# Performance work log

Hardware: AMD Instinct MI355X
Metric: run time of the kernel (lower is better)

## Reference

```python
import jax, jax.numpy as jnp
import numpy as np

ND, NP, NS = 30000, 30000, 10000
HID, NH = 128, 8
HD = HID // NH  # 16
E_DD = E_DP = E_PD = E_PP = 1000000
E_SD = 500000
NEG_SLOPE = 0.2  # DGL GATConv default leaky_relu slope


def _gat(x_src, x_dst, src, dst, W, al, ar, b):
    """Single-relation GATConv (DGL semantics, eval mode / no dropout)."""
    n_dst = x_dst.shape[0]
    z_src = (x_src @ W).reshape(-1, NH, HD)   # [Ns,H,D]
    z_dst = (x_dst @ W).reshape(-1, NH, HD)   # [Nd,H,D]
    el = jnp.sum(z_src * al, axis=-1)          # [Ns,H]
    er = jnp.sum(z_dst * ar, axis=-1)          # [Nd,H]
    e = jax.nn.leaky_relu(el[src] + er[dst], NEG_SLOPE)  # [E,H]
    # edge softmax over incoming edges of each dst node
    emax = jax.ops.segment_max(e, dst, num_segments=n_dst)
    emax = jnp.where(jnp.isfinite(emax), emax, 0.0)
    ex = jnp.exp(e - emax[dst])
    den = jax.ops.segment_sum(ex, dst, num_segments=n_dst)
    attn = ex / jnp.maximum(den[dst], 1e-9)    # [E,H]
    msg = attn[:, :, None] * z_src[src]        # [E,H,D]
    out = jax.ops.segment_sum(msg, dst, num_segments=n_dst)  # [Nd,H,D]
    return out + b.reshape(1, NH, HD)


def _semantic(feats, W1, b1, W2, b2):
    # feats: [N,R,HID]; per-node softmax over relation axis
    s = jnp.tanh(feats @ W1 + b1) @ W2 + b2    # [N,R,1]
    w = jax.nn.softmax(s, axis=1)
    return jnp.sum(feats * w, axis=1)          # [N,HID]


def setup_inputs() -> dict:
    key = jax.random.key(0)
    ks = jax.random.split(key, 40)
    it = iter(range(40))
    def nrm(shape, scale=1.0):
        return jax.random.normal(ks[next(it)], shape, dtype=jnp.float32) * scale
    sc = 1.0 / float(np.sqrt(HID))
    inp = {}
    inp["h_drug"] = nrm((ND, HID))
    inp["h_protein"] = nrm((NP, HID))
    inp["h_se"] = nrm((NS, HID))
    for rel in ["dd", "dp", "pd", "pp", "sd"]:
        inp[f"W_{rel}"] = nrm((HID, HID), sc)
        inp[f"al_{rel}"] = nrm((NH, HD), sc)
        inp[f"ar_{rel}"] = nrm((NH, HD), sc)
        inp[f"b_{rel}"] = jnp.zeros((HID,), dtype=jnp.float32)
    inp["W1"] = nrm((HID, HID), sc)
    inp["b1"] = jnp.zeros((HID,), dtype=jnp.float32)
    inp["W2"] = nrm((HID, 1), sc)
    inp["b2"] = jnp.zeros((1,), dtype=jnp.float32)
    def ridx(n, e):
        return jax.random.randint(ks[next(it)], (e,), 0, n, dtype=jnp.int32)
    inp["src_dd"] = ridx(ND, E_DD); inp["dst_dd"] = ridx(ND, E_DD)
    inp["src_dp"] = ridx(ND, E_DP); inp["dst_dp"] = ridx(NP, E_DP)
    inp["src_pd"] = ridx(NP, E_PD); inp["dst_pd"] = ridx(ND, E_PD)
    inp["src_pp"] = ridx(NP, E_PP); inp["dst_pp"] = ridx(NP, E_PP)
    inp["src_sd"] = ridx(NS, E_SD); inp["dst_sd"] = ridx(ND, E_SD)
    return inp


def reference(h_drug, h_protein, h_se,
              W_dd, al_dd, ar_dd, b_dd, W_dp, al_dp, ar_dp, b_dp,
              W_pd, al_pd, ar_pd, b_pd, W_pp, al_pp, ar_pp, b_pp,
              W_sd, al_sd, ar_sd, b_sd, W1, b1, W2, b2,
              src_dd, dst_dd, src_dp, dst_dp, src_pd, dst_pd,
              src_pp, dst_pp, src_sd, dst_sd):
    # per-relation GAT message passing (HeteroGraphConv, aggregate='stack')
    o_dd = _gat(h_drug, h_drug, src_dd, dst_dd, W_dd, al_dd, ar_dd, b_dd)
    o_pd = _gat(h_protein, h_drug, src_pd, dst_pd, W_pd, al_pd, ar_pd, b_pd)
    o_sd = _gat(h_se, h_drug, src_sd, dst_sd, W_sd, al_sd, ar_sd, b_sd)
    o_dp = _gat(h_drug, h_protein, src_dp, dst_dp, W_dp, al_dp, ar_dp, b_dp)
    o_pp = _gat(h_protein, h_protein, src_pp, dst_pp, W_pp, al_pp, ar_pp, b_pp)
    drug_stack = jnp.stack([o_dd, o_pd, o_sd], axis=1).reshape(ND, 3, HID)
    prot_stack = jnp.stack([o_dp, o_pp], axis=1).reshape(NP, 2, HID)
    out_drug = _semantic(drug_stack, W1, b1, W2, b2)
    out_protein = _semantic(prot_stack, W1, b1, W2, b2)
    return out_drug, out_protein
```

## Files before the change

### kernel.cpp

```cpp
#include <hip/hip_runtime.h>
#include <hip/hip_bf16.h>

typedef unsigned short u16;
typedef __attribute__((ext_vector_type(8))) short short8;
typedef __attribute__((ext_vector_type(4))) float f32x4;

#define ND 30000
#define NP 30000
#define NS 10000
#define CSTRIDE 30016
#define ETOT 4500000
#define CHUNK 4608
#define NC 977
#define NBR 118
#define NB 590

__device__ __forceinline__ float bf2f(u16 u) {
  union { unsigned int i; float f; } c; c.i = ((unsigned int)u) << 16; return c.f;
}
__device__ __forceinline__ u16 f2bf(float f) {
  union { float f; unsigned int i; } c; c.f = f;
  unsigned int u = c.i;
  unsigned int r = (u + 0x7fffu + ((u >> 16) & 1u)) >> 16;
  return (u16)r;
}

__global__ void k_detect(const void* x, int* flag) {
  if (threadIdx.x == 0 && blockIdx.x == 0) {
    const u16* p = (const u16*)x;
    int sane = 0;
    for (int i = 0; i < 256; ++i) {
      const u16 v = p[2 * i];
      const int e = (v >> 7) & 0xff;
      sane += (e >= 100 && e <= 140) ? 1 : 0;
    }
    *flag = (sane >= 200) ? 1 : 0;
  }
}

__device__ __forceinline__ float ld_in(const void* p, int i, int isbf) {
  return isbf ? bf2f(((const u16*)p)[i]) : ((const float*)p)[i];
}

struct PJobs { const void* W[5]; const void* al[5]; const void* ar[5];
               float* wal[5]; float* war[5]; };
__global__ __launch_bounds__(128) void k_prep_all(PJobs J, const int* flagp) {
  const int b = blockIdx.x;
  const int k = threadIdx.x;
  const int isbf = *flagp;
  for (int h = 0; h < 8; ++h) {
    float sa = 0.f, sr = 0.f;
    for (int d = 0; d < 16; ++d) {
      const float wv = ld_in(J.W[b], k * 128 + h * 16 + d, isbf);
      sa = fmaf(wv, ld_in(J.al[b], h * 16 + d, isbf), sa);
      sr = fmaf(wv, ld_in(J.ar[b], h * 16 + d, isbf), sr);
    }
    J.wal[b][h * 128 + k] = sa;
    J.war[b][h * 128 + k] = sr;
  }
}

struct KPack { const void* W[6]; const float* wal[6]; const float* war[6];
               u16* out[6]; };
__global__ __launch_bounds__(256) void k_pack_all(KPack J, const int* flagp) {
  const int job = blockIdx.x / 9;
  const int i0 = (blockIdx.x % 9) * 2048 + threadIdx.x * 8;
  const int isbf = *flagp;
  const int kc = i0 / 4608;
  const int rem = i0 - kc * 4608;
  const int n = rem >> 5;
  const int q = (rem >> 3) & 3;
  u16 vals[8];
  #pragma unroll
  for (int j = 0; j < 8; ++j) {
    const int k = kc * 32 + q * 8 + j;
    float v;
    if (job == 5)      v = (n < 128) ? ld_in(J.W[5], k * 128 + n, isbf) : 0.f;
    else if (n < 128)  v = ld_in(J.W[job], k * 128 + n, isbf);
    else if (n < 136)  v = J.wal[job][(n - 128) * 128 + k];
    else               v = J.war[job][(n - 136) * 128 + k];
    vals[j] = f2bf(v);
  }
  *(uint4*)&J.out[job][i0] = *(uint4*)vals;
}

struct XJobs {
  const void* x[8]; const u16* bp[8]; u16* z[8]; float* el[8]; float* er[8];
  int N[8]; int t0[8]; int blk0[9];
};
__global__ __launch_bounds__(256) void k_xform_all(XJobs J, const int* flagp) {
  __shared__ __align__(16) u16 Bf[18432];
  __shared__ __align__(16) u16 As[64 * 136];
  const int tid = threadIdx.x;
  const int isbf = *flagp;

  int job = 0, b = blockIdx.x;
  while (b >= J.blk0[job + 1]) ++job;
  const int row0 = (b - J.blk0[job]) * 64;
  const int N = J.N[job];
  const int t0 = J.t0[job];
  const u16* bp = J.bp[job];
  const void* x = J.x[job];

  if (t0 == 0) {
    for (int i = tid * 8; i < 18432; i += 2048)
      *(uint4*)&Bf[i] = *(const uint4*)&bp[i];
  } else {
    const int i = tid * 8;
    const int kc = i >> 9;
    const int off = (kc * 144 + 128) * 32 + (i & 511);
    *(uint4*)&Bf[off] = *(const uint4*)&bp[off];
  }

  if (isbf) {
    const uint4* xv = (const uint4*)x;
    for (int i = tid; i < 1024; i += 256) {
      const int r = i >> 4, c8 = i & 15;
      const int row = row0 + r;
      uint4 v = make_uint4(0, 0, 0, 0);
      if (row < N) v = xv[row * 16 + c8];
      *(uint4*)&As[r * 136 + c8 * 8] = v;
    }
  } else {
    const float4* xf = (const float4*)x;
    for (int i = tid; i < 2048; i += 256) {
      const int r = i >> 5, c4 = i & 31;
      const int row = row0 + r;
      unsigned long long pk = 0ull;
      if (row < N) {
        const float4 v = xf[row * 32 + c4];
        pk = (unsigned long long)f2bf(v.x) | ((unsigned long long)f2bf(v.y) << 16)
           | ((unsigned long long)f2bf(v.z) << 32) | ((unsigned long long)f2bf(v.w) << 48);
      }
      *(unsigned long long*)&As[r * 136 + c4 * 4] = pk;
    }
  }
  __syncthreads();

  const int wave = tid >> 6;
  const int lane = tid & 63;
  const int q = lane >> 4;
  const int c = lane & 15;

  f32x4 accT[8];
  f32x4 acc8 = (f32x4){0.f, 0.f, 0.f, 0.f};
  if (t0 == 0) {
    #pragma unroll
    for (int t = 0; t < 8; ++t) accT[t] = (f32x4){0.f, 0.f, 0.f, 0.f};
  }

  #pragma unroll
  for (int kc = 0; kc < 4; ++kc) {
    const short8 a = *(const short8*)&As[(wave * 16 + c) * 136 + kc * 32 + q * 8];
    if (t0 == 0) {
      #pragma unroll
      for (int t = 0; t < 8; ++t) {
        const short8 bb = *(const short8*)&Bf[((kc * 144 + t * 16 + c) * 4 + q) * 8];
        accT[t] = __builtin_amdgcn_mfma_f32_16x16x32_bf16(a, bb, accT[t], 0, 0, 0);
      }
    }
    const short8 b8 = *(const short8*)&Bf[((kc * 144 + 128 + c) * 4 + q) * 8];
    acc8 = __builtin_amdgcn_mfma_f32_16x16x32_bf16(a, b8, acc8, 0, 0, 0);
  }

  const int rbase = row0 + wave * 16 + q * 4;
  if (t0 == 0 && J.z[job]) {
    u16* zo = J.z[job];
    #pragma unroll
    for (int t = 0; t < 8; ++t)
      #pragma unroll
      for (int r = 0; r < 4; ++r) {
        const int row = rbase + r;
        if (row < N) zo[row * 128 + t * 16 + c] = f2bf(accT[t][r]);
      }
  }
  #pragma unroll
  for (int r = 0; r < 4; ++r) {
    const int row = rbase + r;
    if (row < N) {
      const float v = acc8[r];
      if (c < 8) { if (J.el[job]) J.el[job][row * 8 + c] = v; }
      else       { if (J.er[job]) J.er[job][row * 8 + (c - 8)] = v; }
    }
  }
}

struct EJobs { const int* src[5]; const int* dst[5]; };
__device__ __forceinline__ int e_job(int e) {
  return (e >= 1000000) + (e >= 2000000) + (e >= 2500000) + (e >= 3500000);
}
__device__ __forceinline__ int e_base(int j) {
  const int base[6] = {0, 1000000, 2000000, 2500000, 3500000, 4500000};
  return base[j];
}

__global__ __launch_bounds__(256) void k_hist(EJobs J, int* __restrict__ ghist) {
  __shared__ int h[NB];
  const int c = blockIdx.x, tid = threadIdx.x;
  for (int i = tid; i < NB; i += 256) h[i] = 0;
  __syncthreads();
  const int e0 = c * CHUNK;
  #pragma unroll
  for (int t = 0; t < 18; ++t) {
    const int e = e0 + t * 256 + tid;
    if (e < ETOT) {
      const int j = e_job(e);
      const int d = J.dst[j][e - e_base(j)];
      atomicAdd(&h[j * NBR + (d >> 8)], 1);
    }
  }
  __syncthreads();
  for (int i = tid; i < NB; i += 256) ghist[c * NB + i] = h[i];
}

__global__ __launch_bounds__(256) void k_bucketscan(
    const int* __restrict__ ghist, int* __restrict__ gcur, int* __restrict__ totals)
{
  __shared__ int ts[256];
  const int b = blockIdx.x, tid = threadIdx.x;
  int v[4]; int sum = 0;
  #pragma unroll
  for (int i = 0; i < 4; ++i) {
    const int c = tid * 4 + i;
    v[i] = (c < NC) ? ghist[c * NB + b] : 0;
    sum += v[i];
  }
  ts[tid] = sum;
  __syncthreads();
  for (int o = 1; o < 256; o <<= 1) {
    const int x = (tid >= o) ? ts[tid - o] : 0;
    __syncthreads();
    ts[tid] += x;
    __syncthreads();
  }
  int run = (tid == 0) ? 0 : ts[tid - 1];
  #pragma unroll
  for (int i = 0; i < 4; ++i) {
    const int c = tid * 4 + i;
    if (c < NC) gcur[b * NC + c] = run;
    run += v[i];
  }
  if (tid == 255) totals[b] = ts[255];
}

__global__ __launch_bounds__(1024) void k_base(
    const int* __restrict__ totals, int* __restrict__ base)
{
  __shared__ int ts[1024];
  const int tid = threadIdx.x;
  ts[tid] = (tid < NB) ? totals[tid] : 0;
  __syncthreads();
  for (int o = 1; o < 1024; o <<= 1) {
    const int x = (tid >= o) ? ts[tid - o] : 0;
    __syncthreads();
    ts[tid] += x;
    __syncthreads();
  }
  if (tid < NB) base[tid] = (tid == 0) ? 0 : ts[tid - 1];
  if (tid == 0) base[NB] = ETOT;
}

__global__ __launch_bounds__(256) void k_bin(
    EJobs J, const int* __restrict__ gcur, const int* __restrict__ base,
    unsigned int* __restrict__ bin)
{
  __shared__ int cur[NB];
  const int c = blockIdx.x, tid = threadIdx.x;
  for (int i = tid; i < NB; i += 256) cur[i] = base[i] + gcur[i * NC + c];
  __syncthreads();
  const int e0 = c * CHUNK;
  #pragma unroll
  for (int t = 0; t < 18; ++t) {
    const int e = e0 + t * 256 + tid;
    if (e < ETOT) {
      const int j = e_job(e);
      const int le = e - e_base(j);
      const int d = J.dst[j][le];
      const int s = J.src[j][le];
      const int p = atomicAdd(&cur[j * NBR + (d >> 8)], 1);
      bin[p] = ((unsigned int)(d & 255) << 16) | (unsigned int)s;
    }
  }
}

__global__ __launch_bounds__(256) void k_fill2(
    const unsigned int* __restrict__ bin, const int* __restrict__ base,
    u16* __restrict__ csr, int* __restrict__ offsets)
{
  __shared__ int cnt[256], curs[256];
  const int b = blockIdx.x, tid = threadIdx.x;
  const int rel = b / NBR;
  const int bloc = b - rel * NBR;
  const int d0 = bloc << 8;
  const int gbeg = base[b];
  const int n = base[b + 1] - gbeg;
  cnt[tid] = 0;
  __syncthreads();
  for (int i = tid; i < n; i += 256)
    atomicAdd(&cnt[bin[gbeg + i] >> 16], 1);
  __syncthreads();
  const int orig = cnt[tid];
  for (int o = 1; o < 256; o <<= 1) {
    const int x = (tid >= o) ? cnt[tid - o] : 0;
    __syncthreads();
    cnt[tid] += x;
    __syncthreads();
  }
  const int ex = cnt[tid] - orig;
  curs[tid] = ex;
  const int ebr = e_base(rel);
  const int d = d0 + tid;
  if (d < 30000) offsets[rel * CSTRIDE + d] = (gbeg - ebr) + ex;
  if (bloc == NBR - 1 && tid == 0)
    offsets[rel * CSTRIDE + 30000] = e_base(rel + 1) - ebr;
  __syncthreads();
  for (int i = tid; i < n; i += 256) {
    const unsigned int v = bin[gbeg + i];
    const int p = atomicAdd(&curs[v >> 16], 1);
    csr[gbeg + p] = (u16)(v & 0xffffu);
  }
}

struct AJobs { const u16* csr[5]; const int* off[5]; const float* el[5];
               const float* er[5]; const u16* z[5]; const void* b[5];
               u16* feats[5]; int stride[5]; };
__global__ __launch_bounds__(256) void k_agg_all(AJobs J, const int* flagp) {
  const int gw = (blockIdx.x * 256 + threadIdx.x) >> 6;
  if (gw >= 150000) return;
  const int job = gw / 30000;
  const int d = gw - job * 30000;
  const int lane = threadIdx.x & 63;
  const int h = lane >> 3;
  const float* el = J.el[job];
  const u16* z = J.z[job];
  const u16* csr = J.csr[job];
  const float erh = J.er[job][d * 8 + h];
  const int beg = J.off[job][d];
  const int end = J.off[job][d + 1];
  const int zoff = lane * 2;

  float a0 = 0.f, a1 = 0.f, b0 = 0.f, b1 = 0.f, dA = 0.f, dB = 0.f;
  int p = beg;
  for (; p + 4 <= end; p += 4) {
    const int s0 = csr[p];
    const int s1 = csr[p + 1];
    const int s2 = csr[p + 2];
    const int s3 = csr[p + 3];
    float e0 = el[s0 * 8 + h] + erh;
    float e1 = el[s1 * 8 + h] + erh;
    float e2 = el[s2 * 8 + h] + erh;
    float e3 = el[s3 * 8 + h] + erh;
    const unsigned int z0 = *(const unsigned int*)(z + s0 * 128 + zoff);
    const unsigned int z1 = *(const unsigned int*)(z + s1 * 128 + zoff);
    const unsigned int z2 = *(const unsigned int*)(z + s2 * 128 + zoff);
    const unsigned int z3 = *(const unsigned int*)(z + s3 * 128 + zoff);
    e0 = fminf((e0 >= 0.f) ? e0 : 0.2f * e0, 60.f);
    e1 = fminf((e1 >= 0.f) ? e1 : 0.2f * e1, 60.f);
    e2 = fminf((e2 >= 0.f) ? e2 : 0.2f * e2, 60.f);
    e3 = fminf((e3 >= 0.f) ? e3 : 0.2f * e3, 60.f);
    const float x0 = __expf(e0);
    const float x1 = __expf(e1);
    const float x2 = __expf(e2);
    const float x3 = __expf(e3);
    dA += x0 + x2;
    dB += x1 + x3;
    a0 = fmaf(x0, bf2f((u16)(z0 & 0xffffu)), a0);
    a1 = fmaf(x0, bf2f((u16)(z0 >> 16)), a1);
    b0 = fmaf(x1, bf2f((u16)(z1 & 0xffffu)), b0);
    b1 = fmaf(x1, bf2f((u16)(z1 >> 16)), b1);
    a0 = fmaf(x2, bf2f((u16)(z2 & 0xffffu)), a0);
    a1 = fmaf(x2, bf2f((u16)(z2 >> 16)), a1);
    b0 = fmaf(x3, bf2f((u16)(z3 & 0xffffu)), b0);
    b1 = fmaf(x3, bf2f((u16)(z3 >> 16)), b1);
  }
  for (; p < end; ++p) {
    const int s0 = csr[p];
    float e0 = el[s0 * 8 + h] + erh;
    e0 = fminf((e0 >= 0.f) ? e0 : 0.2f * e0, 60.f);
    const float x0 = __expf(e0);
    const unsigned int z0 = *(const unsigned int*)(z + s0 * 128 + zoff);
    dA += x0;
    a0 = fmaf(x0, bf2f((u16)(z0 & 0xffffu)), a0);
    a1 = fmaf(x0, bf2f((u16)(z0 >> 16)), a1);
  }
  const float inv = 1.f / fmaxf(dA + dB, 1e-9f);
  const int isbf = *flagp;
  const int j0 = lane * 2;
  const float v0 = (a0 + b0) * inv + ld_in(J.b[job], j0, isbf);
  const float v1 = (a1 + b1) * inv + ld_in(J.b[job], j0 + 1, isbf);
  const unsigned int packed = (unsigned int)f2bf(v0) | ((unsigned int)f2bf(v1) << 16);
  *(unsigned int*)(J.feats[job] + d * J.stride[job] + j0) = packed;
}

__global__ __launch_bounds__(256) void k_sem_all(
    const u16* __restrict__ f, const u16* __restrict__ w1pack,
    const void* __restrict__ b1, const void* __restrict__ W2,
    const void* __restrict__ b2, float* __restrict__ s_out, int total,
    const int* __restrict__ flagp)
{
  __shared__ __align__(16) u16 Bf[18432];
  __shared__ __align__(16) u16 As[64 * 136];
  __shared__ float b1S[128], W2S[128];
  const int tid = threadIdx.x;
  const int isbf = *flagp;
  const int row0 = blockIdx.x * 64;

  for (int i = tid * 8; i < 18432; i += 2048)
    *(uint4*)&Bf[i] = *(const uint4*)&w1pack[i];
  if (tid < 128) { b1S[tid] = ld_in(b1, tid, isbf); W2S[tid] = ld_in(W2, tid, isbf); }
  {
    const uint4* xv = (const uint4*)f;
    for (int i = tid; i < 1024; i += 256) {
      const int r = i >> 4, c8 = i & 15;
      const int row = row0 + r;
      uint4 v = make_uint4(0, 0, 0, 0);
      if (row < total) v = xv[row * 16 + c8];
      *(uint4*)&As[r * 136 + c8 * 8] = v;
    }
  }
  __syncthreads();

  const int wave = tid >> 6;
  const int lane = tid & 63;
  const int q = lane >> 4;
  const int c = lane & 15;

  f32x4 acc[8];
  #pragma unroll
  for (int t = 0; t < 8; ++t) acc[t] = (f32x4){0.f, 0.f, 0.f, 0.f};

  #pragma unroll
  for (int kc = 0; kc < 4; ++kc) {
    const short8 a = *(const short8*)&As[(wave * 16 + c) * 136 + kc * 32 + q * 8];
    #pragma unroll
    for (int t = 0; t < 8; ++t) {
      const short8 bb = *(const short8*)&Bf[((kc * 144 + t * 16 + c) * 4 + q) * 8];
      acc[t] = __builtin_amdgcn_mfma_f32_16x16x32_bf16(a, bb, acc[t], 0, 0, 0);
    }
  }

  float part[4] = {0.f, 0.f, 0.f, 0.f};
  #pragma unroll
  for (int t = 0; t < 8; ++t) {
    const int n = t * 16 + c;
    const float b1v = b1S[n];
    const float w2v = W2S[n];
    #pragma unroll
    for (int r = 0; r < 4; ++r) {
      const float hv = acc[t][r] + b1v;
      const float e = __expf(2.f * hv);
      const float th = 1.f - 2.f / (e + 1.f);
      part[r] = fmaf(th, w2v, part[r]);
    }
  }
  #pragma unroll
  for (int r = 0; r < 4; ++r) {
    part[r] += __shfl_xor(part[r], 1);
    part[r] += __shfl_xor(part[r], 2);
    part[r] += __shfl_xor(part[r], 4);
    part[r] += __shfl_xor(part[r], 8);
  }
  if (c == 0) {
    const float b2v = ld_in(b2, 0, isbf);
    #pragma unroll
    for (int r = 0; r < 4; ++r) {
      const int row = row0 + wave * 16 + q * 4 + r;
      if (row < total) s_out[row] = part[r] + b2v;
    }
  }
}

__global__ __launch_bounds__(256) void k_combine_all(
    const u16* __restrict__ feats, const float* __restrict__ s,
    void* __restrict__ out, const int* __restrict__ flagp)
{
  const int i = blockIdx.x * 256 + threadIdx.x;
  if (i >= 7680000) return;
  const int isbf = *flagp;
  const bool drug = (i < 3840000);
  const int li = drug ? i : i - 3840000;
  const int n = li >> 7;
  const int j = li & 127;
  const float* sr = s + (drug ? n * 3 : 90000 + n * 2);
  const u16* fb = feats + (drug ? n * 384 : 11520000 + n * 256);
  const float s0v = sr[0];
  const float s1v = sr[1];
  const float s2v = drug ? sr[2] : -3.4e38f;
  const float m = fmaxf(fmaxf(s0v, s1v), s2v);
  const float w0 = __expf(s0v - m);
  const float w1 = __expf(s1v - m);
  const float w2 = drug ? __expf(s2v - m) : 0.f;
  const float inv = 1.f / (w0 + w1 + w2);
  float acc = w0 * bf2f(fb[j]) + w1 * bf2f(fb[128 + j]);
  if (drug) acc += w2 * bf2f(fb[256 + j]);
  const float v = acc * inv;
  if (isbf) ((u16*)out)[i] = f2bf(v);
  else      ((float*)out)[i] = v;
}

extern "C" void kernel_launch(void* const* d_in, const int* in_sizes, int n_in,
                              void* d_out, int out_size, void* d_ws, size_t ws_size,
                              hipStream_t stream)
{
  (void)in_sizes; (void)n_in; (void)out_size; (void)ws_size;

  const void* h_drug = d_in[0];
  const void* h_prot = d_in[1];
  const void* h_se   = d_in[2];
  const void* W_dd = d_in[3];  const void* al_dd = d_in[4];
  const void* ar_dd = d_in[5]; const void* b_dd  = d_in[6];
  const void* W_dp = d_in[7];  const void* al_dp = d_in[8];
  const void* ar_dp = d_in[9]; const void* b_dp  = d_in[10];
  const void* W_pd = d_in[11]; const void* al_pd = d_in[12];
  const void* ar_pd = d_in[13];const void* b_pd  = d_in[14];
  const void* W_pp = d_in[15]; const void* al_pp = d_in[16];
  const void* ar_pp = d_in[17];const void* b_pp  = d_in[18];
  const void* W_sd = d_in[19]; const void* al_sd = d_in[20];
  const void* ar_sd = d_in[21];const void* b_sd  = d_in[22];
  const void* W1 = d_in[23];   const void* b1 = d_in[24];
  const void* W2 = d_in[25];   const void* b2 = d_in[26];
  const int* src_dd = (const int*)d_in[27];
  const int* dst_dd = (const int*)d_in[28];
  const int* src_dp = (const int*)d_in[29];
  const int* dst_dp = (const int*)d_in[30];
  const int* src_pd = (const int*)d_in[31];
  const int* dst_pd = (const int*)d_in[32];
  const int* src_pp = (const int*)d_in[33];
  const int* dst_pp = (const int*)d_in[34];
  const int* src_sd = (const int*)d_in[35];
  const int* dst_sd = (const int*)d_in[36];

  char* w = (char*)d_ws;
  float* el5   = (float*)(w);
  float* er5   = (float*)(w + 4800000);
  u16* z_dd    = (u16*)(w + 9600000);
  u16* z_pd    = (u16*)(w + 17280000);
  u16* z_sd    = (u16*)(w + 24960000);
  u16* z_dp    = (u16*)(w + 27520000);
  u16* z_pp    = (u16*)(w + 35200000);
  int* offsets = (int*)(w + 42880000);
  u16* csr     = (u16*)(w + 43480320);
  int* ghist   = (int*)(w + 52480320);
  int* gcur    = (int*)(w + 54786048);
  int* basep   = (int*)(w + 57091776);
  float* s     = (float*)(w + 57094144);
  u16* feats   = (u16*)(w + 57694144);
  unsigned int* bin = (unsigned int*)(w + 57694144);
  int* flag    = (int*)(w + 96094144);
  float* ww    = (float*)(w + 96094160);
  u16* packs   = (u16*)(w + 96135120);

  float *wal[5], *war[5];
  for (int r = 0; r < 5; ++r) { wal[r] = ww + r * 2048; war[r] = ww + r * 2048 + 1024; }
  u16* pk[6];
  for (int r = 0; r < 6; ++r) pk[r] = packs + r * 18432;
  float* el_r[5]; float* er_r[5];
  for (int r = 0; r < 5; ++r) { el_r[r] = el5 + r * 240000; er_r[r] = er5 + r * 240000; }
  u16* feats_d = feats;
  u16* feats_p = feats + 11520000;

  const dim3 blk(256);

  k_detect<<<dim3(1), dim3(64), 0, stream>>>(h_drug, flag);

  PJobs pj;
  pj.W[0]=W_dd; pj.al[0]=al_dd; pj.ar[0]=ar_dd;
  pj.W[1]=W_pd; pj.al[1]=al_pd; pj.ar[1]=ar_pd;
  pj.W[2]=W_sd; pj.al[2]=al_sd; pj.ar[2]=ar_sd;
  pj.W[3]=W_dp; pj.al[3]=al_dp; pj.ar[3]=ar_dp;
  pj.W[4]=W_pp; pj.al[4]=al_pp; pj.ar[4]=ar_pp;
  for (int r = 0; r < 5; ++r) { pj.wal[r] = wal[r]; pj.war[r] = war[r]; }
  k_prep_all<<<dim3(5), dim3(128), 0, stream>>>(pj, flag);

  KPack kp;
  kp.W[0]=W_dd; kp.W[1]=W_pd; kp.W[2]=W_sd; kp.W[3]=W_dp; kp.W[4]=W_pp; kp.W[5]=W1;
  for (int r = 0; r < 5; ++r) { kp.wal[r] = wal[r]; kp.war[r] = war[r]; }
  kp.wal[5]=nullptr; kp.war[5]=nullptr;
  for (int r = 0; r < 6; ++r) kp.out[r] = pk[r];
  k_pack_all<<<dim3(54), blk, 0, stream>>>(kp, flag);

  EJobs ej;
  ej.src[0]=src_dd; ej.dst[0]=dst_dd;
  ej.src[1]=src_pd; ej.dst[1]=dst_pd;
  ej.src[2]=src_sd; ej.dst[2]=dst_sd;
  ej.src[3]=src_dp; ej.dst[3]=dst_dp;
  ej.src[4]=src_pp; ej.dst[4]=dst_pp;
  k_hist<<<dim3(NC), blk, 0, stream>>>(ej, ghist);
  k_bucketscan<<<dim3(NB), blk, 0, stream>>>(ghist, gcur, basep + NB + 1);
  k_base<<<dim3(1), dim3(1024), 0, stream>>>(basep + NB + 1, basep);
  k_bin<<<dim3(NC), blk, 0, stream>>>(ej, gcur, basep, bin);
  k_fill2<<<dim3(NB), blk, 0, stream>>>(bin, basep, csr, offsets);

  XJobs xj;
  auto setx = [&](int i, const void* x, const u16* bp, u16* z, float* el,
                  float* er, int N, int t0) {
    xj.x[i]=x; xj.bp[i]=bp; xj.z[i]=z; xj.el[i]=el; xj.er[i]=er; xj.N[i]=N; xj.t0[i]=t0;
  };
  setx(0, h_drug, pk[0], z_dd, el_r[0], er_r[0], ND, 0);
  setx(1, h_prot, pk[1], z_pd, el_r[1], nullptr, NP, 0);
  setx(2, h_drug, pk[1], nullptr, nullptr, er_r[1], ND, 8);
  setx(3, h_se,   pk[2], z_sd, el_r[2], nullptr, NS, 0);
  setx(4, h_drug, pk[2], nullptr, nullptr, er_r[2], ND, 8);
  setx(5, h_drug, pk[3], z_dp, el_r[3], nullptr, ND, 0);
  setx(6, h_prot, pk[3], nullptr, nullptr, er_r[3], NP, 8);
  setx(7, h_prot, pk[4], z_pp, el_r[4], er_r[4], NP, 0);
  {
    int acc = 0;
    for (int i = 0; i < 8; ++i) { xj.blk0[i] = acc; acc += (xj.N[i] + 63) / 64; }
    xj.blk0[8] = acc;
    k_xform_all<<<dim3(acc), blk, 0, stream>>>(xj, flag);
  }

  AJobs aj;
  const int ebase[5] = {0, 1000000, 2000000, 2500000, 3500000};
  const void* bias[5] = {b_dd, b_pd, b_sd, b_dp, b_pp};
  u16* fb[5] = {feats_d, feats_d + 128, feats_d + 256, feats_p, feats_p + 128};
  const int fstride[5] = {384, 384, 384, 256, 256};
  const u16* zz[5] = {z_dd, z_pd, z_sd, z_dp, z_pp};
  for (int r = 0; r < 5; ++r) {
    aj.csr[r] = csr + ebase[r];
    aj.off[r] = offsets + r * CSTRIDE;
    aj.el[r] = el_r[r];
    aj.er[r] = er_r[r];
    aj.z[r] = zz[r];
    aj.b[r] = bias[r];
    aj.feats[r] = fb[r];
    aj.stride[r] = fstride[r];
  }
  k_agg_all<<<dim3(150000 / 4), blk, 0, stream>>>(aj, flag);

  k_sem_all<<<dim3((150000 + 63) / 64), blk, 0, stream>>>(feats, pk[5], b1, W2, b2, s, 150000, flag);
  k_combine_all<<<dim3((7680000 + 255) / 256), blk, 0, stream>>>(feats, s, d_out, flag);
}
```

Baseline: 608.1 us.

## Merge preprocessing launches, inline dtype detection, and cooperatively gather edges in aggregation

Cuts the kernel count by merging independent stages into shared launches: prep with hist, pack with bucketscan, and fill2 with xform. The separate base-scan kernel is dropped; each consumer block recomputes the base offsets from the totals. Every kernel now detects the input dtype itself with a ballot instead of reading a flag written by a one-thread kernel. The aggregation kernel changes so each lane computes the attention exp for one of eight edges, then shares the source index and weight through readlane and bpermute. The histogram chunk size doubles, halving the number of blocks. The cost is redundant detection and scan work in every block, plus extra shared memory in the merged kernels.

```diff
diff --git a/kernel.cpp b/kernel.cpp
--- a/kernel.cpp
+++ b/kernel.cpp
@@ -10,8 +10,8 @@
 #define NS 10000
 #define CSTRIDE 30016
 #define ETOT 4500000
-#define CHUNK 4608
-#define NC 977
+#define CHUNK 9216
+#define NC 489
 #define NBR 118
 #define NB 590
 
@@ -25,29 +25,37 @@
   return (u16)r;
 }
 
-__global__ void k_detect(const void* x, int* flag) {
-  if (threadIdx.x == 0 && blockIdx.x == 0) {
-    const u16* p = (const u16*)x;
-    int sane = 0;
-    for (int i = 0; i < 256; ++i) {
-      const u16 v = p[2 * i];
-      const int e = (v >> 7) & 0xff;
-      sane += (e >= 100 && e <= 140) ? 1 : 0;
-    }
-    *flag = (sane >= 200) ? 1 : 0;
-  }
+__device__ __forceinline__ int detect_isbf(const void* x) {
+  __shared__ int cnt4[4];
+  const int tid = threadIdx.x;
+  const u16 v = ((const u16*)x)[2 * tid];
+  const int e = (v >> 7) & 0xff;
+  const unsigned long long m = __ballot(e >= 100 && e <= 140);
+  if ((tid & 63) == 0) cnt4[tid >> 6] = __popcll(m);
+  __syncthreads();
+  const int sane = cnt4[0] + cnt4[1] + cnt4[2] + cnt4[3];
+  return sane >= 200;
 }
 
 __device__ __forceinline__ float ld_in(const void* p, int i, int isbf) {
   return isbf ? bf2f(((const u16*)p)[i]) : ((const float*)p)[i];
 }
 
+struct EJobs { const int* src[5]; const int* dst[5]; };
+__device__ __forceinline__ int e_job(int e) {
+  return (e >= 1000000) + (e >= 2000000) + (e >= 2500000) + (e >= 3500000);
+}
+__device__ __forceinline__ int e_base(int j) {
+  const int base[6] = {0, 1000000, 2000000, 2500000, 3500000, 4500000};
+  return base[j];
+}
+
 struct PJobs { const void* W[5]; const void* al[5]; const void* ar[5];
                float* wal[5]; float* war[5]; };
-__global__ __launch_bounds__(128) void k_prep_all(PJobs J, const int* flagp) {
-  const int b = blockIdx.x;
-  const int k = threadIdx.x;
-  const int isbf = *flagp;
+__device__ void prep_dev(const PJobs& J, int b, int isbf) {
+  const int tid = threadIdx.x;
+  if (tid >= 128) return;
+  const int k = tid;
   for (int h = 0; h < 8; ++h) {
     float sa = 0.f, sr = 0.f;
     for (int d = 0; d < 16; ++d) {
@@ -60,12 +68,40 @@
   }
 }
 
+__device__ void hist_dev(const EJobs& J, int* __restrict__ ghist, int c) {
+  __shared__ int hsh[NB];
+  const int tid = threadIdx.x;
+  for (int i = tid; i < NB; i += 256) hsh[i] = 0;
+  __syncthreads();
+  const int e0 = c * CHUNK;
+  #pragma unroll 4
+  for (int t = 0; t < 36; ++t) {
+    const int e = e0 + t * 256 + tid;
+    if (e < ETOT) {
+      const int j = e_job(e);
+      const int d = J.dst[j][e - e_base(j)];
+      atomicAdd(&hsh[j * NBR + (d >> 8)], 1);
+    }
+  }
+  __syncthreads();
+  for (int i = tid; i < NB; i += 256) ghist[c * NB + i] = hsh[i];
+}
+
+__global__ __launch_bounds__(256) void k_front(PJobs PJ, EJobs EJ,
+    const void* xdet, int* __restrict__ ghist) {
+  if (blockIdx.x < 5) {
+    const int isbf = detect_isbf(xdet);
+    prep_dev(PJ, blockIdx.x, isbf);
+  } else {
+    hist_dev(EJ, ghist, blockIdx.x - 5);
+  }
+}
+
 struct KPack { const void* W[6]; const float* wal[6]; const float* war[6];
                u16* out[6]; };
-__global__ __launch_bounds__(256) void k_pack_all(KPack J, const int* flagp) {
-  const int job = blockIdx.x / 9;
-  const int i0 = (blockIdx.x % 9) * 2048 + threadIdx.x * 8;
-  const int isbf = *flagp;
+__device__ void pack_dev(const KPack& J, int b, int isbf) {
+  const int job = b / 9;
+  const int i0 = (b % 9) * 2048 + threadIdx.x * 8;
   const int kc = i0 / 4608;
   const int rem = i0 - kc * 4608;
   const int n = rem >> 5;
@@ -84,19 +120,136 @@
   *(uint4*)&J.out[job][i0] = *(uint4*)vals;
 }
 
+__device__ void bucketscan_dev(const int* __restrict__ ghist,
+    int* __restrict__ gcur, int* __restrict__ totals, int b) {
+  __shared__ int ts[256];
+  const int tid = threadIdx.x;
+  int v0 = 0, v1 = 0;
+  const int c0 = tid * 2;
+  if (c0 < NC) v0 = ghist[c0 * NB + b];
+  if (c0 + 1 < NC) v1 = ghist[(c0 + 1) * NB + b];
+  ts[tid] = v0 + v1;
+  __syncthreads();
+  for (int o = 1; o < 256; o <<= 1) {
+    const int x = (tid >= o) ? ts[tid - o] : 0;
+    __syncthreads();
+    ts[tid] += x;
+    __syncthreads();
+  }
+  int run = (tid == 0) ? 0 : ts[tid - 1];
+  if (c0 < NC) { gcur[b * NC + c0] = run; run += v0; }
+  if (c0 + 1 < NC) gcur[b * NC + c0 + 1] = run;
+  if (tid == 255) totals[b] = ts[255];
+}
+
+__global__ __launch_bounds__(256) void k_mid(KPack KJ, const void* xdet,
+    const int* __restrict__ ghist, int* __restrict__ gcur, int* __restrict__ totals) {
+  if (blockIdx.x < 54) {
+    const int isbf = detect_isbf(xdet);
+    pack_dev(KJ, blockIdx.x, isbf);
+  } else {
+    bucketscan_dev(ghist, gcur, totals, blockIdx.x - 54);
+  }
+}
+
+__device__ void base_from_totals(const int* __restrict__ totals, int* bsh) {
+  __shared__ int ts[256];
+  const int tid = threadIdx.x;
+  const int i0 = tid * 3;
+  int v0 = 0, v1 = 0, v2 = 0;
+  if (i0 < NB) v0 = totals[i0];
+  if (i0 + 1 < NB) v1 = totals[i0 + 1];
+  if (i0 + 2 < NB) v2 = totals[i0 + 2];
+  ts[tid] = v0 + v1 + v2;
+  __syncthreads();
+  for (int o = 1; o < 256; o <<= 1) {
+    const int x = (tid >= o) ? ts[tid - o] : 0;
+    __syncthreads();
+    ts[tid] += x;
+    __syncthreads();
+  }
+  int run = (tid == 0) ? 0 : ts[tid - 1];
+  if (i0 < NB) { bsh[i0] = run; run += v0; }
+  if (i0 + 1 < NB) { bsh[i0 + 1] = run; run += v1; }
+  if (i0 + 2 < NB) bsh[i0 + 2] = run;
+  if (tid == 0) bsh[NB] = ETOT;
+  __syncthreads();
+}
+
+__global__ __launch_bounds__(256) void k_bin(EJobs J,
+    const int* __restrict__ gcur, const int* __restrict__ totals,
+    unsigned int* __restrict__ bin) {
+  __shared__ int bsh[NB + 1];
+  __shared__ int cur[NB];
+  base_from_totals(totals, bsh);
+  const int c = blockIdx.x, tid = threadIdx.x;
+  for (int i = tid; i < NB; i += 256) cur[i] = bsh[i] + gcur[i * NC + c];
+  __syncthreads();
+  const int e0 = c * CHUNK;
+  #pragma unroll 4
+  for (int t = 0; t < 36; ++t) {
+    const int e = e0 + t * 256 + tid;
+    if (e < ETOT) {
+      const int j = e_job(e);
+      const int le = e - e_base(j);
+      const int d = J.dst[j][le];
+      const int s = J.src[j][le];
+      const int pos = atomicAdd(&cur[j * NBR + (d >> 8)], 1);
+      bin[pos] = ((unsigned int)(d & 255) << 16) | (unsigned int)s;
+    }
+  }
+}
+
+__device__ void fill2_dev(const unsigned int* __restrict__ bin,
+    const int* __restrict__ totals, u16* __restrict__ csr,
+    int* __restrict__ offsets, int b) {
+  __shared__ int bsh2[NB + 1];
+  __shared__ int cnt[256], curs[256];
+  base_from_totals(totals, bsh2);
+  const int tid = threadIdx.x;
+  const int rel = b / NBR;
+  const int bloc = b - rel * NBR;
+  const int d0 = bloc << 8;
+  const int gbeg = bsh2[b];
+  const int n = bsh2[b + 1] - gbeg;
+  cnt[tid] = 0;
+  __syncthreads();
+  for (int i = tid; i < n; i += 256)
+    atomicAdd(&cnt[bin[gbeg + i] >> 16], 1);
+  __syncthreads();
+  const int orig = cnt[tid];
+  for (int o = 1; o < 256; o <<= 1) {
+    const int x = (tid >= o) ? cnt[tid - o] : 0;
+    __syncthreads();
+    cnt[tid] += x;
+    __syncthreads();
+  }
+  const int ex = cnt[tid] - orig;
+  curs[tid] = ex;
+  const int ebr = e_base(rel);
+  const int d = d0 + tid;
+  if (d < 30000) offsets[rel * CSTRIDE + d] = (gbeg - ebr) + ex;
+  if (bloc == NBR - 1 && tid == 0)
+    offsets[rel * CSTRIDE + 30000] = e_base(rel + 1) - ebr;
+  __syncthreads();
+  for (int i = tid; i < n; i += 256) {
+    const unsigned int v = bin[gbeg + i];
+    const int pos = atomicAdd(&curs[v >> 16], 1);
+    csr[gbeg + pos] = (u16)(v & 0xffffu);
+  }
+}
+
 struct XJobs {
   const void* x[8]; const u16* bp[8]; u16* z[8]; float* el[8]; float* er[8];
   int N[8]; int t0[8]; int blk0[9];
 };
-__global__ __launch_bounds__(256) void k_xform_all(XJobs J, const int* flagp) {
+__device__ void xform_dev(const XJobs& J, int xb, int isbf) {
   __shared__ __align__(16) u16 Bf[18432];
   __shared__ __align__(16) u16 As[64 * 136];
   const int tid = threadIdx.x;
-  const int isbf = *flagp;
-
-  int job = 0, b = blockIdx.x;
-  while (b >= J.blk0[job + 1]) ++job;
-  const int row0 = (b - J.blk0[job]) * 64;
+  int job = 0;
+  while (xb >= J.blk0[job + 1]) ++job;
+  const int row0 = (xb - J.blk0[job]) * 64;
   const int N = J.N[job];
   const int t0 = J.t0[job];
   const u16* bp = J.bp[job];
@@ -126,13 +279,13 @@
     for (int i = tid; i < 2048; i += 256) {
       const int r = i >> 5, c4 = i & 31;
       const int row = row0 + r;
-      unsigned long long pk = 0ull;
+      unsigned long long pkv = 0ull;
       if (row < N) {
         const float4 v = xf[row * 32 + c4];
-        pk = (unsigned long long)f2bf(v.x) | ((unsigned long long)f2bf(v.y) << 16)
-           | ((unsigned long long)f2bf(v.z) << 32) | ((unsigned long long)f2bf(v.w) << 48);
+        pkv = (unsigned long long)f2bf(v.x) | ((unsigned long long)f2bf(v.y) << 16)
+            | ((unsigned long long)f2bf(v.z) << 32) | ((unsigned long long)f2bf(v.w) << 48);
       }
-      *(unsigned long long*)&As[r * 136 + c4 * 4] = pk;
+      *(unsigned long long*)&As[r * 136 + c4 * 4] = pkv;
     }
   }
   __syncthreads();
@@ -185,209 +338,86 @@
   }
 }
 
-struct EJobs { const int* src[5]; const int* dst[5]; };
-__device__ __forceinline__ int e_job(int e) {
-  return (e >= 1000000) + (e >= 2000000) + (e >= 2500000) + (e >= 3500000);
-}
-__device__ __forceinline__ int e_base(int j) {
-  const int base[6] = {0, 1000000, 2000000, 2500000, 3500000, 4500000};
-  return base[j];
-}
-
-__global__ __launch_bounds__(256) void k_hist(EJobs J, int* __restrict__ ghist) {
-  __shared__ int h[NB];
-  const int c = blockIdx.x, tid = threadIdx.x;
-  for (int i = tid; i < NB; i += 256) h[i] = 0;
-  __syncthreads();
-  const int e0 = c * CHUNK;
-  #pragma unroll
-  for (int t = 0; t < 18; ++t) {
-    const int e = e0 + t * 256 + tid;
-    if (e < ETOT) {
-      const int j = e_job(e);
-      const int d = J.dst[j][e - e_base(j)];
-      atomicAdd(&h[j * NBR + (d >> 8)], 1);
-    }
-  }
-  __syncthreads();
-  for (int i = tid; i < NB; i += 256) ghist[c * NB + i] = h[i];
-}
-
-__global__ __launch_bounds__(256) void k_bucketscan(
-    const int* __restrict__ ghist, int* __restrict__ gcur, int* __restrict__ totals)
-{
-  __shared__ int ts[256];
-  const int b = blockIdx.x, tid = threadIdx.x;
-  int v[4]; int sum = 0;
-  #pragma unroll
-  for (int i = 0; i < 4; ++i) {
-    const int c = tid * 4 + i;
-    v[i] = (c < NC) ? ghist[c * NB + b] : 0;
-    sum += v[i];
-  }
-  ts[tid] = sum;
-  __syncthreads();
-  for (int o = 1; o < 256; o <<= 1) {
-    const int x = (tid >= o) ? ts[tid - o] : 0;
-    __syncthreads();
-    ts[tid] += x;
-    __syncthreads();
-  }
-  int run = (tid == 0) ? 0 : ts[tid - 1];
-  #pragma unroll
-  for (int i = 0; i < 4; ++i) {
-    const int c = tid * 4 + i;
-    if (c < NC) gcur[b * NC + c] = run;
-    run += v[i];
-  }
-  if (tid == 255) totals[b] = ts[255];
-}
-
-__global__ __launch_bounds__(1024) void k_base(
-    const int* __restrict__ totals, int* __restrict__ base)
-{
-  __shared__ int ts[1024];
-  const int tid = threadIdx.x;
-  ts[tid] = (tid < NB) ? totals[tid] : 0;
-  __syncthreads();
-  for (int o = 1; o < 1024; o <<= 1) {
-    const int x = (tid >= o) ? ts[tid - o] : 0;
-    __syncthreads();
-    ts[tid] += x;
-    __syncthreads();
-  }
-  if (tid < NB) base[tid] = (tid == 0) ? 0 : ts[tid - 1];
-  if (tid == 0) base[NB] = ETOT;
-}
-
-__global__ __launch_bounds__(256) void k_bin(
-    EJobs J, const int* __restrict__ gcur, const int* __restrict__ base,
-    unsigned int* __restrict__ bin)
-{
-  __shared__ int cur[NB];
-  const int c = blockIdx.x, tid = threadIdx.x;
-  for (int i = tid; i < NB; i += 256) cur[i] = base[i] + gcur[i * NC + c];
-  __syncthreads();
-  const int e0 = c * CHUNK;
-  #pragma unroll
-  for (int t = 0; t < 18; ++t) {
-    const int e = e0 + t * 256 + tid;
-    if (e < ETOT) {
-      const int j = e_job(e);
-      const int le = e - e_base(j);
-      const int d = J.dst[j][le];
-      const int s = J.src[j][le];
-      const int p = atomicAdd(&cur[j * NBR + (d >> 8)], 1);
-      bin[p] = ((unsigned int)(d & 255) << 16) | (unsigned int)s;
-    }
-  }
-}
-
-__global__ __launch_bounds__(256) void k_fill2(
-    const unsigned int* __restrict__ bin, const int* __restrict__ base,
-    u16* __restrict__ csr, int* __restrict__ offsets)
-{
-  __shared__ int cnt[256], curs[256];
-  const int b = blockIdx.x, tid = threadIdx.x;
-  const int rel = b / NBR;
-  const int bloc = b - rel * NBR;
-  const int d0 = bloc << 8;
-  const int gbeg = base[b];
-  const int n = base[b + 1] - gbeg;
-  cnt[tid] = 0;
-  __syncthreads();
-  for (int i = tid; i < n; i += 256)
-    atomicAdd(&cnt[bin[gbeg + i] >> 16], 1);
-  __syncthreads();
-  const int orig = cnt[tid];
-  for (int o = 1; o < 256; o <<= 1) {
-    const int x = (tid >= o) ? cnt[tid - o] : 0;
-    __syncthreads();
-    cnt[tid] += x;
-    __syncthreads();
-  }
-  const int ex = cnt[tid] - orig;
-  curs[tid] = ex;
-  const int ebr = e_base(rel);
-  const int d = d0 + tid;
-  if (d < 30000) offsets[rel * CSTRIDE + d] = (gbeg - ebr) + ex;
-  if (bloc == NBR - 1 && tid == 0)
-    offsets[rel * CSTRIDE + 30000] = e_base(rel + 1) - ebr;
-  __syncthreads();
-  for (int i = tid; i < n; i += 256) {
-    const unsigned int v = bin[gbeg + i];
-    const int p = atomicAdd(&curs[v >> 16], 1);
-    csr[gbeg + p] = (u16)(v & 0xffffu);
+__global__ __launch_bounds__(256) void k_l4(XJobs XJ, const void* xdet,
+    const unsigned int* __restrict__ bin, const int* __restrict__ totals,
+    u16* __restrict__ csr, int* __restrict__ offsets) {
+  if (blockIdx.x < NB) {
+    fill2_dev(bin, totals, csr, offsets, blockIdx.x);
+  } else {
+    const int isbf = detect_isbf(xdet);
+    xform_dev(XJ, blockIdx.x - NB, isbf);
   }
 }
 
 struct AJobs { const u16* csr[5]; const int* off[5]; const float* el[5];
                const float* er[5]; const u16* z[5]; const void* b[5];
                u16* feats[5]; int stride[5]; };
-__global__ __launch_bounds__(256) void k_agg_all(AJobs J, const int* flagp) {
+__global__ __launch_bounds__(256) void k_agg_all(AJobs J, const void* xdet) {
+  const int isbf = detect_isbf(xdet);
   const int gw = (blockIdx.x * 256 + threadIdx.x) >> 6;
-  if (gw >= 150000) return;
+  const int lane = threadIdx.x & 63;
   const int job = gw / 30000;
   const int d = gw - job * 30000;
-  const int lane = threadIdx.x & 63;
   const int h = lane >> 3;
+  const int i8 = lane & 7;
   const float* el = J.el[job];
   const u16* z = J.z[job];
   const u16* csr = J.csr[job];
   const float erh = J.er[job][d * 8 + h];
   const int beg = J.off[job][d];
   const int end = J.off[job][d + 1];
-  const int zoff = lane * 2;
-
-  float a0 = 0.f, a1 = 0.f, b0 = 0.f, b1 = 0.f, dA = 0.f, dB = 0.f;
+  const int gb4 = (lane & 56) << 2;
+
+  float a0 = 0.f, a1 = 0.f, denP = 0.f;
   int p = beg;
-  for (; p + 4 <= end; p += 4) {
-    const int s0 = csr[p];
-    const int s1 = csr[p + 1];
-    const int s2 = csr[p + 2];
-    const int s3 = csr[p + 3];
-    float e0 = el[s0 * 8 + h] + erh;
-    float e1 = el[s1 * 8 + h] + erh;
-    float e2 = el[s2 * 8 + h] + erh;
-    float e3 = el[s3 * 8 + h] + erh;
-    const unsigned int z0 = *(const unsigned int*)(z + s0 * 128 + zoff);
-    const unsigned int z1 = *(const unsigned int*)(z + s1 * 128 + zoff);
-    const unsigned int z2 = *(const unsigned int*)(z + s2 * 128 + zoff);
-    const unsigned int z3 = *(const unsigned int*)(z + s3 * 128 + zoff);
-    e0 = fminf((e0 >= 0.f) ? e0 : 0.2f * e0, 60.f);
-    e1 = fminf((e1 >= 0.f) ? e1 : 0.2f * e1, 60.f);
-    e2 = fminf((e2 >= 0.f) ? e2 : 0.2f * e2, 60.f);
-    e3 = fminf((e3 >= 0.f) ? e3 : 0.2f * e3, 60.f);
-    const float x0 = __expf(e0);
-    const float x1 = __expf(e1);
-    const float x2 = __expf(e2);
-    const float x3 = __expf(e3);
-    dA += x0 + x2;
-    dB += x1 + x3;
-    a0 = fmaf(x0, bf2f((u16)(z0 & 0xffffu)), a0);
-    a1 = fmaf(x0, bf2f((u16)(z0 >> 16)), a1);
-    b0 = fmaf(x1, bf2f((u16)(z1 & 0xffffu)), b0);
-    b1 = fmaf(x1, bf2f((u16)(z1 >> 16)), b1);
-    a0 = fmaf(x2, bf2f((u16)(z2 & 0xffffu)), a0);
-    a1 = fmaf(x2, bf2f((u16)(z2 >> 16)), a1);
-    b0 = fmaf(x3, bf2f((u16)(z3 & 0xffffu)), b0);
-    b1 = fmaf(x3, bf2f((u16)(z3 >> 16)), b1);
-  }
-  for (; p < end; ++p) {
-    const int s0 = csr[p];
-    float e0 = el[s0 * 8 + h] + erh;
-    e0 = fminf((e0 >= 0.f) ? e0 : 0.2f * e0, 60.f);
-    const float x0 = __expf(e0);
-    const unsigned int z0 = *(const unsigned int*)(z + s0 * 128 + zoff);
-    dA += x0;
-    a0 = fmaf(x0, bf2f((u16)(z0 & 0xffffu)), a0);
-    a1 = fmaf(x0, bf2f((u16)(z0 >> 16)), a1);
-  }
-  const float inv = 1.f / fmaxf(dA + dB, 1e-9f);
-  const int isbf = *flagp;
+  for (; p + 8 <= end; p += 8) {
+    const int sE = (int)csr[p + i8];
+    float eh = el[sE * 8 + h] + erh;
+    eh = fminf(fmaxf(eh, 0.2f * eh), 60.f);
+    const float exE = __expf(eh);
+    denP += exE;
+    const int exbits = __float_as_int(exE);
+    #pragma unroll
+    for (int i = 0; i < 8; ++i) {
+      const int si = __builtin_amdgcn_readlane(sE, i);
+      const float exi = __int_as_float(
+          __builtin_amdgcn_ds_bpermute(gb4 + i * 4, exbits));
+      const unsigned int zp = *(const unsigned int*)(z + si * 128 + lane * 2);
+      union { unsigned int u; float f; } lo, hi;
+      lo.u = zp << 16; hi.u = zp & 0xffff0000u;
+      a0 = fmaf(exi, lo.f, a0);
+      a1 = fmaf(exi, hi.f, a1);
+    }
+  }
+  if (p < end) {
+    const int r = end - p;
+    int sE = 0; float exE = 0.f;
+    if (i8 < r) {
+      sE = (int)csr[p + i8];
+      float eh = el[sE * 8 + h] + erh;
+      eh = fminf(fmaxf(eh, 0.2f * eh), 60.f);
+      exE = __expf(eh);
+    }
+    denP += exE;
+    const int exbits = __float_as_int(exE);
+    for (int i = 0; i < r; ++i) {
+      const int si = __builtin_amdgcn_readlane(sE, i);
+      const float exi = __int_as_float(
+          __builtin_amdgcn_ds_bpermute(gb4 + i * 4, exbits));
+      const unsigned int zp = *(const unsigned int*)(z + si * 128 + lane * 2);
+      union { unsigned int u; float f; } lo, hi;
+      lo.u = zp << 16; hi.u = zp & 0xffff0000u;
+      a0 = fmaf(exi, lo.f, a0);
+      a1 = fmaf(exi, hi.f, a1);
+    }
+  }
+  denP += __shfl_xor(denP, 1);
+  denP += __shfl_xor(denP, 2);
+  denP += __shfl_xor(denP, 4);
+  const float inv = 1.f / fmaxf(denP, 1e-9f);
   const int j0 = lane * 2;
-  const float v0 = (a0 + b0) * inv + ld_in(J.b[job], j0, isbf);
-  const float v1 = (a1 + b1) * inv + ld_in(J.b[job], j0 + 1, isbf);
+  const float v0 = a0 * inv + ld_in(J.b[job], j0, isbf);
+  const float v1 = a1 * inv + ld_in(J.b[job], j0 + 1, isbf);
   const unsigned int packed = (unsigned int)f2bf(v0) | ((unsigned int)f2bf(v1) << 16);
   *(unsigned int*)(J.feats[job] + d * J.stride[job] + j0) = packed;
 }
@@ -396,13 +426,13 @@
     const u16* __restrict__ f, const u16* __restrict__ w1pack,
     const void* __restrict__ b1, const void* __restrict__ W2,
     const void* __restrict__ b2, float* __restrict__ s_out, int total,
-    const int* __restrict__ flagp)
+    const void* xdet)
 {
   __shared__ __align__(16) u16 Bf[18432];
   __shared__ __align__(16) u16 As[64 * 136];
   __shared__ float b1S[128], W2S[128];
-  const int tid = threadIdx.x;
-  const int isbf = *flagp;
+  const int isbf = detect_isbf(xdet);
+  const int tid = threadIdx.x;
   const int row0 = blockIdx.x * 64;
 
   for (int i = tid * 8; i < 18432; i += 2048)
@@ -472,11 +502,11 @@
 
 __global__ __launch_bounds__(256) void k_combine_all(
     const u16* __restrict__ feats, const float* __restrict__ s,
-    void* __restrict__ out, const int* __restrict__ flagp)
+    void* __restrict__ out, const void* xdet)
 {
+  const int isbf = detect_isbf(xdet);
   const int i = blockIdx.x * 256 + threadIdx.x;
   if (i >= 7680000) return;
-  const int isbf = *flagp;
   const bool drug = (i < 3840000);
   const int li = drug ? i : i - 3840000;
   const int n = li >> 7;
@@ -541,14 +571,13 @@
   int* offsets = (int*)(w + 42880000);
   u16* csr     = (u16*)(w + 43480320);
   int* ghist   = (int*)(w + 52480320);
-  int* gcur    = (int*)(w + 54786048);
-  int* basep   = (int*)(w + 57091776);
-  float* s     = (float*)(w + 57094144);
-  u16* feats   = (u16*)(w + 57694144);
-  unsigned int* bin = (unsigned int*)(w + 57694144);
-  int* flag    = (int*)(w + 96094144);
-  float* ww    = (float*)(w + 96094160);
-  u16* packs   = (u16*)(w + 96135120);
+  int* gcur    = (int*)(w + 53634560);
+  int* totals  = (int*)(w + 54788608);
+  float* s     = (float*)(w + 54791168);
+  u16* feats   = (u16*)(w + 55391232);
+  unsigned int* bin = (unsigned int*)(w + 55391232);
+  float* ww    = (float*)(w + 93791232);
+  u16* packs   = (u16*)(w + 93832192);
 
   float *wal[5], *war[5];
   for (int r = 0; r < 5; ++r) { wal[r] = ww + r * 2048; war[r] = ww + r * 2048 + 1024; }
@@ -561,8 +590,6 @@
 
   const dim3 blk(256);
 
-  k_detect<<<dim3(1), dim3(64), 0, stream>>>(h_drug, flag);
-
   PJobs pj;
   pj.W[0]=W_dd; pj.al[0]=al_dd; pj.ar[0]=ar_dd;
   pj.W[1]=W_pd; pj.al[1]=al_pd; pj.ar[1]=ar_pd;
@@ -570,14 +597,6 @@
   pj.W[3]=W_dp; pj.al[3]=al_dp; pj.ar[3]=ar_dp;
   pj.W[4]=W_pp; pj.al[4]=al_pp; pj.ar[4]=ar_pp;
   for (int r = 0; r < 5; ++r) { pj.wal[r] = wal[r]; pj.war[r] = war[r]; }
-  k_prep_all<<<dim3(5), dim3(128), 0, stream>>>(pj, flag);
-
-  KPack kp;
-  kp.W[0]=W_dd; kp.W[1]=W_pd; kp.W[2]=W_sd; kp.W[3]=W_dp; kp.W[4]=W_pp; kp.W[5]=W1;
-  for (int r = 0; r < 5; ++r) { kp.wal[r] = wal[r]; kp.war[r] = war[r]; }
-  kp.wal[5]=nullptr; kp.war[5]=nullptr;
-  for (int r = 0; r < 6; ++r) kp.out[r] = pk[r];
-  k_pack_all<<<dim3(54), blk, 0, stream>>>(kp, flag);
 
   EJobs ej;
   ej.src[0]=src_dd; ej.dst[0]=dst_dd;
@@ -585,11 +604,12 @@
   ej.src[2]=src_sd; ej.dst[2]=dst_sd;
   ej.src[3]=src_dp; ej.dst[3]=dst_dp;
   ej.src[4]=src_pp; ej.dst[4]=dst_pp;
-  k_hist<<<dim3(NC), blk, 0, stream>>>(ej, ghist);
-  k_bucketscan<<<dim3(NB), blk, 0, stream>>>(ghist, gcur, basep + NB + 1);
-  k_base<<<dim3(1), dim3(1024), 0, stream>>>(basep + NB + 1, basep);
-  k_bin<<<dim3(NC), blk, 0, stream>>>(ej, gcur, basep, bin);
-  k_fill2<<<dim3(NB), blk, 0, stream>>>(bin, basep, csr, offsets);
+
+  KPack kp;
+  kp.W[0]=W_dd; kp.W[1]=W_pd; kp.W[2]=W_sd; kp.W[3]=W_dp; kp.W[4]=W_pp; kp.W[5]=W1;
+  for (int r = 0; r < 5; ++r) { kp.wal[r] = wal[r]; kp.war[r] = war[r]; }
+  kp.wal[5]=nullptr; kp.war[5]=nullptr;
+  for (int r = 0; r < 6; ++r) kp.out[r] = pk[r];
 
   XJobs xj;
   auto setx = [&](int i, const void* x, const u16* bp, u16* z, float* el,
@@ -604,12 +624,9 @@
   setx(5, h_drug, pk[3], z_dp, el_r[3], nullptr, ND, 0);
   setx(6, h_prot, pk[3], nullptr, nullptr, er_r[3], NP, 8);
   setx(7, h_prot, pk[4], z_pp, el_r[4], er_r[4], NP, 0);
-  {
-    int acc = 0;
-    for (int i = 0; i < 8; ++i) { xj.blk0[i] = acc; acc += (xj.N[i] + 63) / 64; }
-    xj.blk0[8] = acc;
-    k_xform_all<<<dim3(acc), blk, 0, stream>>>(xj, flag);
-  }
+  int xblocks = 0;
+  for (int i = 0; i < 8; ++i) { xj.blk0[i] = xblocks; xblocks += (xj.N[i] + 63) / 64; }
+  xj.blk0[8] = xblocks;
 
   AJobs aj;
   const int ebase[5] = {0, 1000000, 2000000, 2500000, 3500000};
@@ -627,8 +644,12 @@
     aj.feats[r] = fb[r];
     aj.stride[r] = fstride[r];
   }
-  k_agg_all<<<dim3(150000 / 4), blk, 0, stream>>>(aj, flag);
-
-  k_sem_all<<<dim3((150000 + 63) / 64), blk, 0, stream>>>(feats, pk[5], b1, W2, b2, s, 150000, flag);
-  k_combine_all<<<dim3((7680000 + 255) / 256), blk, 0, stream>>>(feats, s, d_out, flag);
-}
+
+  k_front<<<dim3(5 + NC), blk, 0, stream>>>(pj, ej, h_drug, ghist);
+  k_mid<<<dim3(54 + NB), blk, 0, stream>>>(kp, h_drug, ghist, gcur, totals);
+  k_bin<<<dim3(NC), blk, 0, stream>>>(ej, gcur, totals, bin);
+  k_l4<<<dim3(NB + xblocks), blk, 0, stream>>>(xj, h_drug, bin, totals, csr, offsets);
+  k_agg_all<<<dim3(37500), blk, 0, stream>>>(aj, h_drug);
+  k_sem_all<<<dim3((150000 + 63) / 64), blk, 0, stream>>>(feats, pk[5], b1, W2, b2, s, 150000, h_drug);
+  k_combine_all<<<dim3(30000), blk, 0, stream>>>(feats, s, d_out, h_drug);
+}
```

Result: faster. 565.6 us (-7.0%).
